# Kernel tuning notes

Hardware: AMD Instinct MI355X
Metric: run time of the kernel (lower is better)

The kernel has to match this reference:

```python
import jax, jax.numpy as jnp
import numpy as np

B, T, C = 2, 2048, 1024
H = 16
HD = C // H  # head_dim = 64


def setup_inputs() -> dict:
    key = jax.random.key(0)
    ks = jax.random.split(key, 5)
    s = 0.02
    return {
        "x": jax.random.normal(ks[0], (B, T, C), dtype=jnp.float32),
        "Wqkv": jax.random.normal(ks[1], (C, 3 * C), dtype=jnp.float32) * s,
        "bqkv": jax.random.normal(ks[2], (3 * C,), dtype=jnp.float32) * s,
        "Wproj": jax.random.normal(ks[3], (C, C), dtype=jnp.float32) * s,
        "bproj": jax.random.normal(ks[4], (C,), dtype=jnp.float32) * s,
    }


def reference(x, Wqkv, bqkv, Wproj, bproj):
    b, t, c = x.shape
    qkv = x @ Wqkv + bqkv  # [B,T,3C]
    q, k, v = jnp.split(qkv, 3, axis=-1)
    # [B,T,C] -> [B,H,T,HD]
    q = q.reshape(b, t, H, HD).transpose(0, 2, 1, 3)
    k = k.reshape(b, t, H, HD).transpose(0, 2, 1, 3)
    v = v.reshape(b, t, H, HD).transpose(0, 2, 1, 3)
    scale = 1.0 / jnp.sqrt(jnp.float32(HD))
    att = jnp.einsum('bhqd,bhkd->bhqk', q, k) * scale  # [B,H,T,T]
    causal = jnp.tril(jnp.ones((t, t), dtype=bool))
    att = jnp.where(causal[None, None], att, jnp.float32(-jnp.inf))
    att = jax.nn.softmax(att, axis=-1)
    y = jnp.einsum('bhqk,bhkd->bhqd', att, v)  # [B,H,T,HD]
    y = y.transpose(0, 2, 1, 3).reshape(b, t, c)
    return y @ Wproj + bproj
```

## Files before the change

### kernel.cpp

```cpp
#include <hip/hip_runtime.h>

typedef unsigned short u16;
typedef __attribute__((ext_vector_type(4))) float f32x4;
typedef __attribute__((ext_vector_type(8))) short short8;

#define AS1 __attribute__((address_space(1)))
#define AS3 __attribute__((address_space(3)))

#define B_  2
#define T_  2048
#define C_  1024
#define H_  16
#define HD_ 64
#define N3C 3072
#define BT_ 4096

__device__ __forceinline__ u16 f2bf(float x) {
    unsigned u = __float_as_uint(x);
    u += 0x7fff + ((u >> 16) & 1);
    return (u16)(u >> 16);
}

__global__ __launch_bounds__(256)
void conv_all(const float* __restrict__ x, u16* __restrict__ xb,
              const float* __restrict__ Wq, u16* __restrict__ WqT,
              const float* __restrict__ Wp, u16* __restrict__ WpT) {
    __shared__ float tile[64][68];
    const int tid = threadIdx.x;
    const int b = blockIdx.x;
    if (b < 4096) {
        int i = b * 256 + tid;
        float4 f = ((const float4*)x)[i];
        ushort4 o;
        o.x = f2bf(f.x); o.y = f2bf(f.y); o.z = f2bf(f.z); o.w = f2bf(f.w);
        ((ushort4*)xb)[i] = o;
        return;
    }
    const float* W; u16* WT; int N, k0, n0;
    if (b < 4096 + 768) {
        int bb = b - 4096; W = Wq; WT = WqT; N = N3C;
        n0 = (bb % 48) * 64; k0 = (bb / 48) * 64;
    } else {
        int bb = b - 4864; W = Wp; WT = WpT; N = C_;
        n0 = (bb % 16) * 64; k0 = (bb / 16) * 64;
    }
    #pragma unroll
    for (int i = 0; i < 4; ++i) {
        int slot = tid + i * 256;
        int row = slot >> 4, c4 = (slot & 15) * 4;
        *(float4*)&tile[row][c4] = *(const float4*)&W[(size_t)(k0 + row) * N + n0 + c4];
    }
    __syncthreads();
    #pragma unroll
    for (int i = 0; i < 4; ++i) {
        int slot = tid + i * 256;
        int nn = slot >> 4, k4 = (slot & 15) * 4;
        ushort4 o;
        o.x = f2bf(tile[k4 + 0][nn]); o.y = f2bf(tile[k4 + 1][nn]);
        o.z = f2bf(tile[k4 + 2][nn]); o.w = f2bf(tile[k4 + 3][nn]);
        *(ushort4*)&WT[(size_t)(n0 + nn) * 1024 + k0 + k4] = o;
    }
}

__device__ __forceinline__ void gemm_core(const u16* __restrict__ A, const u16* __restrict__ BT,
                                          u16* As, u16* Bs,
                                          int m0, int n0, f32x4 (&acc)[4][4]) {
    const int tid = threadIdx.x;
    const int lane = tid & 63, w = tid >> 6;
    const int l15 = lane & 15, quad = lane >> 4;
    const int row0 = (w >> 1) * 64, col0 = (w & 1) * 64;
    const int srow = lane >> 3;
    const int schunk = (lane & 7) ^ srow;

    auto stage = [&](int buf, int k0) {
        #pragma unroll
        for (int j = 0; j < 4; ++j) {
            int rbase = w * 32 + j * 8;
            const u16* ga = A  + (size_t)(m0 + rbase + srow) * 1024 + k0 + schunk * 8;
            const u16* gb = BT + (size_t)(n0 + rbase + srow) * 1024 + k0 + schunk * 8;
            __builtin_amdgcn_global_load_lds((const AS1 void*)ga,
                (AS3 void*)(As + buf * (128 * 64) + rbase * 64), 16, 0, 0);
            __builtin_amdgcn_global_load_lds((const AS1 void*)gb,
                (AS3 void*)(Bs + buf * (128 * 64) + rbase * 64), 16, 0, 0);
        }
    };

    stage(0, 0);
    #pragma unroll
    for (int it = 0; it < 16; ++it) {
        const int cur = it & 1;
        if (it + 1 < 16) {
            stage(cur ^ 1, (it + 1) * 64);
            asm volatile("s_waitcnt vmcnt(8)\n\ts_barrier" ::: "memory");
        } else {
            asm volatile("s_waitcnt vmcnt(0)\n\ts_barrier" ::: "memory");
        }
        const u16* Ac = As + cur * (128 * 64);
        const u16* Bc = Bs + cur * (128 * 64);
        #pragma unroll
        for (int s = 0; s < 2; ++s) {
            short8 a[4], b[4];
            #pragma unroll
            for (int rt = 0; rt < 4; ++rt) {
                int row = row0 + rt * 16 + l15;
                a[rt] = *(const short8*)&Ac[row * 64 + (((s * 4 + quad) ^ (l15 & 7)) * 8)];
            }
            #pragma unroll
            for (int ct = 0; ct < 4; ++ct) {
                int row = col0 + ct * 16 + l15;
                b[ct] = *(const short8*)&Bc[row * 64 + (((s * 4 + quad) ^ (l15 & 7)) * 8)];
            }
            #pragma unroll
            for (int rt = 0; rt < 4; ++rt)
                #pragma unroll
                for (int ct = 0; ct < 4; ++ct)
                    acc[rt][ct] = __builtin_amdgcn_mfma_f32_16x16x32_bf16(a[rt], b[ct], acc[rt][ct], 0, 0, 0);
        }
        asm volatile("s_waitcnt lgkmcnt(0)\n\ts_barrier" ::: "memory");
    }
}

__global__ __launch_bounds__(256)
void qkv_gemm(const u16* __restrict__ A, const u16* __restrict__ BT,
              const float* __restrict__ bias,
              u16* __restrict__ q, u16* __restrict__ k, u16* __restrict__ vT) {
    __shared__ __align__(16) u16 As[2 * 128 * 64];
    __shared__ __align__(16) u16 Bs[2 * 128 * 64];
    const int m0 = blockIdx.y * 128, n0 = blockIdx.x * 128;
    f32x4 acc[4][4] = {};
    gemm_core(A, BT, As, Bs, m0, n0, acc);

    const int tid = threadIdx.x;
    const int lane = tid & 63, w = tid >> 6;
    const int l15 = lane & 15, quad = lane >> 4;
    const int row0 = (w >> 1) * 64, col0 = (w & 1) * 64;
    const int which = n0 >> 10;

    #pragma unroll
    for (int ct = 0; ct < 4; ++ct) {
        int n = n0 + col0 + ct * 16 + l15;
        int nl = n & 1023, h = nl >> 6, d = nl & 63;
        float bv = bias[n];
        #pragma unroll
        for (int rt = 0; rt < 4; ++rt) {
            int mb = m0 + row0 + rt * 16 + quad * 4;
            int bb = mb >> 11, t0 = mb & 2047;
            f32x4 v4 = acc[rt][ct];
            if (which == 0) {
                size_t base = ((size_t)(bb * H_ + h) * T_ + t0) * HD_ + d;
                #pragma unroll
                for (int r = 0; r < 4; ++r)
                    q[base + (size_t)r * HD_] = f2bf((v4[r] + bv) * 0.125f);
            } else if (which == 1) {
                size_t base = ((size_t)(bb * H_ + h) * T_ + t0) * HD_ + d;
                #pragma unroll
                for (int r = 0; r < 4; ++r)
                    k[base + (size_t)r * HD_] = f2bf(v4[r] + bv);
            } else {
                ushort4 o;
                o.x = f2bf(v4[0] + bv); o.y = f2bf(v4[1] + bv);
                o.z = f2bf(v4[2] + bv); o.w = f2bf(v4[3] + bv);
                *(ushort4*)&vT[((size_t)(bb * H_ + h) * HD_ + d) * T_ + t0] = o;
            }
        }
    }
}

__global__ __launch_bounds__(256)
void attn(const u16* __restrict__ q, const u16* __restrict__ k,
          const u16* __restrict__ vT, u16* __restrict__ y) {
    __shared__ __align__(16) u16 Ks[2 * 64 * 64];
    __shared__ __align__(16) u16 Vs[2 * 64 * 64];
    __shared__ __align__(16) u16 Ps[4 * 16 * 72];
    const int tid = threadIdx.x;
    const int lane = tid & 63, w = tid >> 6;
    const int l15 = lane & 15, quad = lane >> 4;
    const int srow = lane >> 3, schunk = (lane & 7) ^ srow;
    const int idx = blockIdx.x;
    const int bh = idx & 31;
    const int p = idx >> 5;
    const int qtH = 31 - p, qtL = p;
    const u16* qp = q  + (size_t)bh * T_ * HD_;
    const u16* kp = k  + (size_t)bh * T_ * HD_;
    const u16* vp = vT + (size_t)bh * HD_ * T_;
    u16* Pw = Ps + w * 16 * 72;

    const int qrowH = qtH * 64 + w * 16 + l15;
    const int qrowL = qtL * 64 + w * 16 + l15;
    short8 qfH[2], qfL[2];
    #pragma unroll
    for (int s = 0; s < 2; ++s) {
        qfH[s] = *(const short8*)&qp[(size_t)qrowH * HD_ + s * 32 + quad * 8];
        qfL[s] = *(const short8*)&qp[(size_t)qrowL * HD_ + s * 32 + quad * 8];
    }

    auto stage = [&](int buf, int kt) {
        const int kb = kt * 64;
        #pragma unroll
        for (int j = 0; j < 2; ++j) {
            int row = w * 16 + j * 8 + srow;
            __builtin_amdgcn_global_load_lds(
                (const AS1 void*)(kp + (size_t)(kb + row) * HD_ + schunk * 8),
                (AS3 void*)(Ks + buf * (64 * 64) + (w * 16 + j * 8) * 64), 16, 0, 0);
            __builtin_amdgcn_global_load_lds(
                (const AS1 void*)(vp + (size_t)row * T_ + kb + schunk * 8),
                (AS3 void*)(Vs + buf * (64 * 64) + (w * 16 + j * 8) * 64), 16, 0, 0);
        }
    };

    f32x4 oH[4] = {}, oL[4] = {};
    float lH = 0.f, lL = 0.f;
    stage(0, 0);

    for (int kt = 0; kt <= qtH; ++kt) {
        const int kb = kt * 64;
        const int cur = kt & 1;
        if (kt < qtH) {
            stage(cur ^ 1, kt + 1);
            asm volatile("s_waitcnt vmcnt(4)\n\ts_barrier" ::: "memory");
        } else {
            asm volatile("s_waitcnt vmcnt(0)\n\ts_barrier" ::: "memory");
        }
        const u16* Kc = Ks + cur * (64 * 64);
        const u16* Vc = Vs + cur * (64 * 64);

        short8 ka[4][2], va[4][2];
        #pragma unroll
        for (int ct = 0; ct < 4; ++ct)
            #pragma unroll
            for (int s = 0; s < 2; ++s) {
                int xo = ((s * 4 + quad) ^ (l15 & 7)) * 8;
                ka[ct][s] = *(const short8*)&Kc[(ct * 16 + l15) * 64 + xo];
                va[ct][s] = *(const short8*)&Vc[(ct * 16 + l15) * 64 + xo];
            }

        {
            f32x4 st[4] = {};
            #pragma unroll
            for (int s = 0; s < 2; ++s)
                #pragma unroll
                for (int ct = 0; ct < 4; ++ct)
                    st[ct] = __builtin_amdgcn_mfma_f32_16x16x32_bf16(ka[ct][s], qfH[s], st[ct], 0, 0, 0);
            const bool last = (kt == qtH);
            float psum = 0.f;
            #pragma unroll
            for (int ct = 0; ct < 4; ++ct) {
                float pe[4];
                #pragma unroll
                for (int r = 0; r < 4; ++r) {
                    pe[r] = __expf(st[ct][r]);
                    if (last && (kb + ct * 16 + quad * 4 + r) > qrowH) pe[r] = 0.f;
                    psum += pe[r];
                }
                uint2 pk;
                pk.x = (unsigned)f2bf(pe[0]) | ((unsigned)f2bf(pe[1]) << 16);
                pk.y = (unsigned)f2bf(pe[2]) | ((unsigned)f2bf(pe[3]) << 16);
                *(uint2*)&Pw[l15 * 72 + ct * 16 + quad * 4] = pk;
            }
            lH += psum;
            asm volatile("s_waitcnt lgkmcnt(0)" ::: "memory");
            #pragma unroll
            for (int s = 0; s < 2; ++s) {
                short8 pb = *(const short8*)&Pw[l15 * 72 + s * 32 + quad * 8];
                #pragma unroll
                for (int n = 0; n < 4; ++n)
                    oH[n] = __builtin_amdgcn_mfma_f32_16x16x32_bf16(va[n][s], pb, oH[n], 0, 0, 0);
            }
        }
        if (kt <= qtL) {
            f32x4 st[4] = {};
            #pragma unroll
            for (int s = 0; s < 2; ++s)
                #pragma unroll
                for (int ct = 0; ct < 4; ++ct)
                    st[ct] = __builtin_amdgcn_mfma_f32_16x16x32_bf16(ka[ct][s], qfL[s], st[ct], 0, 0, 0);
            const bool last = (kt == qtL);
            float psum = 0.f;
            #pragma unroll
            for (int ct = 0; ct < 4; ++ct) {
                float pe[4];
                #pragma unroll
                for (int r = 0; r < 4; ++r) {
                    pe[r] = __expf(st[ct][r]);
                    if (last && (kb + ct * 16 + quad * 4 + r) > qrowL) pe[r] = 0.f;
                    psum += pe[r];
                }
                uint2 pk;
                pk.x = (unsigned)f2bf(pe[0]) | ((unsigned)f2bf(pe[1]) << 16);
                pk.y = (unsigned)f2bf(pe[2]) | ((unsigned)f2bf(pe[3]) << 16);
                *(uint2*)&Pw[l15 * 72 + ct * 16 + quad * 4] = pk;
            }
            lL += psum;
            asm volatile("s_waitcnt lgkmcnt(0)" ::: "memory");
            #pragma unroll
            for (int s = 0; s < 2; ++s) {
                short8 pb = *(const short8*)&Pw[l15 * 72 + s * 32 + quad * 8];
                #pragma unroll
                for (int n = 0; n < 4; ++n)
                    oL[n] = __builtin_amdgcn_mfma_f32_16x16x32_bf16(va[n][s], pb, oL[n], 0, 0, 0);
            }
        }
        asm volatile("s_waitcnt lgkmcnt(0)\n\ts_barrier" ::: "memory");
    }

    lH += __shfl_xor(lH, 16); lH += __shfl_xor(lH, 32);
    lL += __shfl_xor(lL, 16); lL += __shfl_xor(lL, 32);
    const float invH = 1.f / lH, invL = 1.f / lL;
    const int bb = bh >> 4, h = bh & 15;
    #pragma unroll
    for (int n = 0; n < 4; ++n) {
        uint2 pk;
        pk.x = (unsigned)f2bf(oH[n][0] * invH) | ((unsigned)f2bf(oH[n][1] * invH) << 16);
        pk.y = (unsigned)f2bf(oH[n][2] * invH) | ((unsigned)f2bf(oH[n][3] * invH) << 16);
        *(uint2*)&y[((size_t)(bb * T_ + qrowH)) * C_ + h * 64 + n * 16 + quad * 4] = pk;
        uint2 pl;
        pl.x = (unsigned)f2bf(oL[n][0] * invL) | ((unsigned)f2bf(oL[n][1] * invL) << 16);
        pl.y = (unsigned)f2bf(oL[n][2] * invL) | ((unsigned)f2bf(oL[n][3] * invL) << 16);
        *(uint2*)&y[((size_t)(bb * T_ + qrowL)) * C_ + h * 64 + n * 16 + quad * 4] = pl;
    }
}

__global__ __launch_bounds__(256)
void proj_gemm(const u16* __restrict__ A, const u16* __restrict__ BT,
               const float* __restrict__ bias, float* __restrict__ out) {
    __shared__ __align__(16) u16 As[2 * 128 * 64];
    __shared__ __align__(16) u16 Bs[2 * 128 * 64];
    const int m0 = blockIdx.y * 128, n0 = blockIdx.x * 128;
    f32x4 acc[4][4] = {};
    gemm_core(A, BT, As, Bs, m0, n0, acc);

    const int tid = threadIdx.x;
    const int lane = tid & 63, w = tid >> 6;
    const int l15 = lane & 15, quad = lane >> 4;
    const int row0 = (w >> 1) * 64, col0 = (w & 1) * 64;

    #pragma unroll
    for (int ct = 0; ct < 4; ++ct) {
        int n = n0 + col0 + ct * 16 + l15;
        float bv = bias[n];
        #pragma unroll
        for (int rt = 0; rt < 4; ++rt) {
            int mb = m0 + row0 + rt * 16 + quad * 4;
            f32x4 v4 = acc[rt][ct];
            #pragma unroll
            for (int r = 0; r < 4; ++r)
                out[(size_t)(mb + r) * 1024 + n] = v4[r] + bv;
        }
    }
}

extern "C" void kernel_launch(void* const* d_in, const int* in_sizes, int n_in,
                              void* d_out, int out_size, void* d_ws, size_t ws_size,
                              hipStream_t stream) {
    const float* x     = (const float*)d_in[0];
    const float* Wqkv  = (const float*)d_in[1];
    const float* bqkv  = (const float*)d_in[2];
    const float* Wproj = (const float*)d_in[3];
    const float* bproj = (const float*)d_in[4];

    u16* xb     = (u16*)d_ws;
    u16* WqkvT  = xb + (size_t)4 * 1024 * 1024;
    u16* WprojT = WqkvT + (size_t)3 * 1024 * 1024;
    u16* q      = WprojT + (size_t)1024 * 1024;
    u16* kk     = q + (size_t)4 * 1024 * 1024;
    u16* vT     = kk + (size_t)4 * 1024 * 1024;
    u16* y      = vT + (size_t)4 * 1024 * 1024;

    conv_all<<<5120, 256, 0, stream>>>(x, xb, Wqkv, WqkvT, Wproj, WprojT);
    qkv_gemm<<<dim3(N3C / 128, BT_ / 128), 256, 0, stream>>>(xb, WqkvT, bqkv, q, kk, vT);
    attn<<<512, 256, 0, stream>>>(q, kk, vT, y);
    proj_gemm<<<dim3(C_ / 128, BT_ / 128), 256, 0, stream>>>(y, WprojT, bproj, (float*)d_out);
}
```

Before: 184.5 us.

## Split paired causal attention tiles into one tile per block, use exp2 and packed bf16 cvt

The attention kernel previously paired a high and a low query tile per block to balance causal work across 512 blocks. It now launches 1024 blocks, each handling a single query tile, with heavy tiles ordered first. This raises parallelism and cuts per-block register pressure, at the cost of relying on the hardware scheduler for load balance and loading each K/V tile once per query tile. The change also folds log2(e) into the Q scale so softmax can use exp2f, and replaces manual bf16 rounding with the packed v_cvt_pk_bf16_f32 instruction throughout.

```diff
diff --git a/kernel.cpp b/kernel.cpp
--- a/kernel.cpp
+++ b/kernel.cpp
@@ -21,6 +21,12 @@
     return (u16)(u >> 16);
 }
 
+__device__ __forceinline__ unsigned cvt_pk_bf16(float a, float b) {
+    unsigned r;
+    asm("v_cvt_pk_bf16_f32 %0, %1, %2" : "=v"(r) : "v"(a), "v"(b));
+    return r;
+}
+
 __global__ __launch_bounds__(256)
 void conv_all(const float* __restrict__ x, u16* __restrict__ xb,
               const float* __restrict__ Wq, u16* __restrict__ WqT,
@@ -31,9 +37,10 @@
     if (b < 4096) {
         int i = b * 256 + tid;
         float4 f = ((const float4*)x)[i];
-        ushort4 o;
-        o.x = f2bf(f.x); o.y = f2bf(f.y); o.z = f2bf(f.z); o.w = f2bf(f.w);
-        ((ushort4*)xb)[i] = o;
+        uint2 o;
+        o.x = cvt_pk_bf16(f.x, f.y);
+        o.y = cvt_pk_bf16(f.z, f.w);
+        ((uint2*)xb)[i] = o;
         return;
     }
     const float* W; u16* WT; int N, k0, n0;
@@ -55,10 +62,10 @@
     for (int i = 0; i < 4; ++i) {
         int slot = tid + i * 256;
         int nn = slot >> 4, k4 = (slot & 15) * 4;
-        ushort4 o;
-        o.x = f2bf(tile[k4 + 0][nn]); o.y = f2bf(tile[k4 + 1][nn]);
-        o.z = f2bf(tile[k4 + 2][nn]); o.w = f2bf(tile[k4 + 3][nn]);
-        *(ushort4*)&WT[(size_t)(n0 + nn) * 1024 + k0 + k4] = o;
+        uint2 o;
+        o.x = cvt_pk_bf16(tile[k4 + 0][nn], tile[k4 + 1][nn]);
+        o.y = cvt_pk_bf16(tile[k4 + 2][nn], tile[k4 + 3][nn]);
+        *(uint2*)&WT[(size_t)(n0 + nn) * 1024 + k0 + k4] = o;
     }
 }
 
@@ -135,6 +142,7 @@
     const int l15 = lane & 15, quad = lane >> 4;
     const int row0 = (w >> 1) * 64, col0 = (w & 1) * 64;
     const int which = n0 >> 10;
+    const float QSCALE = 0.125f * 1.4426950408889634f;
 
     #pragma unroll
     for (int ct = 0; ct < 4; ++ct) {
@@ -150,17 +158,17 @@
                 size_t base = ((size_t)(bb * H_ + h) * T_ + t0) * HD_ + d;
                 #pragma unroll
                 for (int r = 0; r < 4; ++r)
-                    q[base + (size_t)r * HD_] = f2bf((v4[r] + bv) * 0.125f);
+                    q[base + (size_t)r * HD_] = f2bf((v4[r] + bv) * QSCALE);
             } else if (which == 1) {
                 size_t base = ((size_t)(bb * H_ + h) * T_ + t0) * HD_ + d;
                 #pragma unroll
                 for (int r = 0; r < 4; ++r)
                     k[base + (size_t)r * HD_] = f2bf(v4[r] + bv);
             } else {
-                ushort4 o;
-                o.x = f2bf(v4[0] + bv); o.y = f2bf(v4[1] + bv);
-                o.z = f2bf(v4[2] + bv); o.w = f2bf(v4[3] + bv);
-                *(ushort4*)&vT[((size_t)(bb * H_ + h) * HD_ + d) * T_ + t0] = o;
+                uint2 o;
+                o.x = cvt_pk_bf16(v4[0] + bv, v4[1] + bv);
+                o.y = cvt_pk_bf16(v4[2] + bv, v4[3] + bv);
+                *(uint2*)&vT[((size_t)(bb * H_ + h) * HD_ + d) * T_ + t0] = o;
             }
         }
     }
@@ -178,21 +186,17 @@
     const int srow = lane >> 3, schunk = (lane & 7) ^ srow;
     const int idx = blockIdx.x;
     const int bh = idx & 31;
-    const int p = idx >> 5;
-    const int qtH = 31 - p, qtL = p;
+    const int qt = 31 - (idx >> 5);
     const u16* qp = q  + (size_t)bh * T_ * HD_;
     const u16* kp = k  + (size_t)bh * T_ * HD_;
     const u16* vp = vT + (size_t)bh * HD_ * T_;
     u16* Pw = Ps + w * 16 * 72;
 
-    const int qrowH = qtH * 64 + w * 16 + l15;
-    const int qrowL = qtL * 64 + w * 16 + l15;
-    short8 qfH[2], qfL[2];
-    #pragma unroll
-    for (int s = 0; s < 2; ++s) {
-        qfH[s] = *(const short8*)&qp[(size_t)qrowH * HD_ + s * 32 + quad * 8];
-        qfL[s] = *(const short8*)&qp[(size_t)qrowL * HD_ + s * 32 + quad * 8];
-    }
+    const int qrow = qt * 64 + w * 16 + l15;
+    short8 qf[2];
+    #pragma unroll
+    for (int s = 0; s < 2; ++s)
+        qf[s] = *(const short8*)&qp[(size_t)qrow * HD_ + s * 32 + quad * 8];
 
     auto stage = [&](int buf, int kt) {
         const int kb = kt * 64;
@@ -208,14 +212,14 @@
         }
     };
 
-    f32x4 oH[4] = {}, oL[4] = {};
-    float lH = 0.f, lL = 0.f;
+    f32x4 o[4] = {};
+    float l = 0.f;
     stage(0, 0);
 
-    for (int kt = 0; kt <= qtH; ++kt) {
+    for (int kt = 0; kt <= qt; ++kt) {
         const int kb = kt * 64;
         const int cur = kt & 1;
-        if (kt < qtH) {
+        if (kt < qt) {
             stage(cur ^ 1, kt + 1);
             asm volatile("s_waitcnt vmcnt(4)\n\ts_barrier" ::: "memory");
         } else {
@@ -234,89 +238,58 @@
                 va[ct][s] = *(const short8*)&Vc[(ct * 16 + l15) * 64 + xo];
             }
 
-        {
-            f32x4 st[4] = {};
-            #pragma unroll
-            for (int s = 0; s < 2; ++s)
+        f32x4 st[4] = {};
+        #pragma unroll
+        for (int s = 0; s < 2; ++s)
+            #pragma unroll
+            for (int ct = 0; ct < 4; ++ct)
+                st[ct] = __builtin_amdgcn_mfma_f32_16x16x32_bf16(ka[ct][s], qf[s], st[ct], 0, 0, 0);
+
+        float pe[16];
+        #pragma unroll
+        for (int ct = 0; ct < 4; ++ct)
+            #pragma unroll
+            for (int r = 0; r < 4; ++r)
+                pe[ct * 4 + r] = exp2f(st[ct][r]);
+        if (kt == qt) {
+            #pragma unroll
+            for (int ct = 0; ct < 4; ++ct)
                 #pragma unroll
-                for (int ct = 0; ct < 4; ++ct)
-                    st[ct] = __builtin_amdgcn_mfma_f32_16x16x32_bf16(ka[ct][s], qfH[s], st[ct], 0, 0, 0);
-            const bool last = (kt == qtH);
-            float psum = 0.f;
-            #pragma unroll
-            for (int ct = 0; ct < 4; ++ct) {
-                float pe[4];
-                #pragma unroll
-                for (int r = 0; r < 4; ++r) {
-                    pe[r] = __expf(st[ct][r]);
-                    if (last && (kb + ct * 16 + quad * 4 + r) > qrowH) pe[r] = 0.f;
-                    psum += pe[r];
-                }
-                uint2 pk;
-                pk.x = (unsigned)f2bf(pe[0]) | ((unsigned)f2bf(pe[1]) << 16);
-                pk.y = (unsigned)f2bf(pe[2]) | ((unsigned)f2bf(pe[3]) << 16);
-                *(uint2*)&Pw[l15 * 72 + ct * 16 + quad * 4] = pk;
-            }
-            lH += psum;
-            asm volatile("s_waitcnt lgkmcnt(0)" ::: "memory");
-            #pragma unroll
-            for (int s = 0; s < 2; ++s) {
-                short8 pb = *(const short8*)&Pw[l15 * 72 + s * 32 + quad * 8];
-                #pragma unroll
-                for (int n = 0; n < 4; ++n)
-                    oH[n] = __builtin_amdgcn_mfma_f32_16x16x32_bf16(va[n][s], pb, oH[n], 0, 0, 0);
-            }
-        }
-        if (kt <= qtL) {
-            f32x4 st[4] = {};
-            #pragma unroll
-            for (int s = 0; s < 2; ++s)
-                #pragma unroll
-                for (int ct = 0; ct < 4; ++ct)
-                    st[ct] = __builtin_amdgcn_mfma_f32_16x16x32_bf16(ka[ct][s], qfL[s], st[ct], 0, 0, 0);
-            const bool last = (kt == qtL);
-            float psum = 0.f;
-            #pragma unroll
-            for (int ct = 0; ct < 4; ++ct) {
-                float pe[4];
-                #pragma unroll
-                for (int r = 0; r < 4; ++r) {
-                    pe[r] = __expf(st[ct][r]);
-                    if (last && (kb + ct * 16 + quad * 4 + r) > qrowL) pe[r] = 0.f;
-                    psum += pe[r];
-                }
-                uint2 pk;
-                pk.x = (unsigned)f2bf(pe[0]) | ((unsigned)f2bf(pe[1]) << 16);
-                pk.y = (unsigned)f2bf(pe[2]) | ((unsigned)f2bf(pe[3]) << 16);
-                *(uint2*)&Pw[l15 * 72 + ct * 16 + quad * 4] = pk;
-            }
-            lL += psum;
-            asm volatile("s_waitcnt lgkmcnt(0)" ::: "memory");
-            #pragma unroll
-            for (int s = 0; s < 2; ++s) {
-                short8 pb = *(const short8*)&Pw[l15 * 72 + s * 32 + quad * 8];
-                #pragma unroll
-                for (int n = 0; n < 4; ++n)
-                    oL[n] = __builtin_amdgcn_mfma_f32_16x16x32_bf16(va[n][s], pb, oL[n], 0, 0, 0);
-            }
+                for (int r = 0; r < 4; ++r)
+                    if ((kb + ct * 16 + quad * 4 + r) > qrow) pe[ct * 4 + r] = 0.f;
+        }
+        float psum = 0.f;
+        #pragma unroll
+        for (int i = 0; i < 16; ++i) psum += pe[i];
+        l += psum;
+        #pragma unroll
+        for (int ct = 0; ct < 4; ++ct) {
+            uint2 pk;
+            pk.x = cvt_pk_bf16(pe[ct * 4 + 0], pe[ct * 4 + 1]);
+            pk.y = cvt_pk_bf16(pe[ct * 4 + 2], pe[ct * 4 + 3]);
+            *(uint2*)&Pw[l15 * 72 + ct * 16 + quad * 4] = pk;
+        }
+        asm volatile("s_waitcnt lgkmcnt(0)" ::: "memory");
+
+        #pragma unroll
+        for (int s = 0; s < 2; ++s) {
+            short8 pb = *(const short8*)&Pw[l15 * 72 + s * 32 + quad * 8];
+            #pragma unroll
+            for (int n = 0; n < 4; ++n)
+                o[n] = __builtin_amdgcn_mfma_f32_16x16x32_bf16(va[n][s], pb, o[n], 0, 0, 0);
         }
         asm volatile("s_waitcnt lgkmcnt(0)\n\ts_barrier" ::: "memory");
     }
 
-    lH += __shfl_xor(lH, 16); lH += __shfl_xor(lH, 32);
-    lL += __shfl_xor(lL, 16); lL += __shfl_xor(lL, 32);
-    const float invH = 1.f / lH, invL = 1.f / lL;
+    l += __shfl_xor(l, 16); l += __shfl_xor(l, 32);
+    const float inv = 1.f / l;
     const int bb = bh >> 4, h = bh & 15;
     #pragma unroll
     for (int n = 0; n < 4; ++n) {
         uint2 pk;
-        pk.x = (unsigned)f2bf(oH[n][0] * invH) | ((unsigned)f2bf(oH[n][1] * invH) << 16);
-        pk.y = (unsigned)f2bf(oH[n][2] * invH) | ((unsigned)f2bf(oH[n][3] * invH) << 16);
-        *(uint2*)&y[((size_t)(bb * T_ + qrowH)) * C_ + h * 64 + n * 16 + quad * 4] = pk;
-        uint2 pl;
-        pl.x = (unsigned)f2bf(oL[n][0] * invL) | ((unsigned)f2bf(oL[n][1] * invL) << 16);
-        pl.y = (unsigned)f2bf(oL[n][2] * invL) | ((unsigned)f2bf(oL[n][3] * invL) << 16);
-        *(uint2*)&y[((size_t)(bb * T_ + qrowL)) * C_ + h * 64 + n * 16 + quad * 4] = pl;
+        pk.x = cvt_pk_bf16(o[n][0] * inv, o[n][1] * inv);
+        pk.y = cvt_pk_bf16(o[n][2] * inv, o[n][3] * inv);
+        *(uint2*)&y[((size_t)(bb * T_ + qrow)) * C_ + h * 64 + n * 16 + quad * 4] = pk;
     }
 }
 
@@ -368,6 +341,6 @@
 
     conv_all<<<5120, 256, 0, stream>>>(x, xb, Wqkv, WqkvT, Wproj, WprojT);
     qkv_gemm<<<dim3(N3C / 128, BT_ / 128), 256, 0, stream>>>(xb, WqkvT, bqkv, q, kk, vT);
-    attn<<<512, 256, 0, stream>>>(q, kk, vT, y);
+    attn<<<1024, 256, 0, stream>>>(q, kk, vT, y);
     proj_gemm<<<dim3(C_ / 128, BT_ / 128), 256, 0, stream>>>(y, WprojT, bproj, (float*)d_out);
 }
```

Result: no change. 182.5 us (-1.1%).
